# Optimization experiments

Measured on AMD Instinct MI355X. Metric: run time of the kernel, lower is better.

## Reference

```python
import jax, jax.numpy as jnp
import numpy as np

B, D, H, G, WR = 8192, 1024, 1024, 2, 64
URANKS = [64, 64]


def setup_inputs() -> dict:
    key = jax.random.key(0)
    ks = jax.random.split(key, 12)
    s = 0.1
    return {
        "x": jax.random.normal(ks[0], (B, D), jnp.float32),
        "h": jax.random.normal(ks[1], (B, H), jnp.float32),
        "c": jax.random.normal(ks[2], (B, H), jnp.float32),
        "dia_x": s * jax.random.normal(ks[3], (1, D), jnp.float32),
        "dia_h": s * jax.random.normal(ks[4], (1, H), jnp.float32),
        "Ux": s * jax.random.normal(ks[5], (D, WR), jnp.float32),
        "Vx": s * jax.random.normal(ks[6], (4 * H, WR), jnp.float32),
        "Uh_0": s * jax.random.normal(ks[7], (G, H // G, URANKS[0]), jnp.float32),
        "Vh_0": s * jax.random.normal(ks[8], (G, URANKS[0], 4 * (H // G)), jnp.float32),
        "Uh_1": s * jax.random.normal(ks[9], (G, H // G, URANKS[1]), jnp.float32),
        "Vh_1": s * jax.random.normal(ks[10], (G, URANKS[1], 4 * (H // G)), jnp.float32),
        "bias_x": jnp.ones((1, 4 * H), jnp.float32),
        "bias_h": jnp.ones((1, 4 * H), jnp.float32),
    }


def reference(x, h, c, dia_x, dia_h, Ux, Vx, Uh_0, Vh_0, Uh_1, Vh_1, bias_x, bias_h):
    Bn, Dn = x.shape
    Hn = h.shape[1]
    g = Uh_0.shape[0]
    Hg = Hn // g
    r0 = Uh_0.shape[2]

    # diagonal (vector-multiplication) paths, x-part zero-padded to hidden width
    vm_x = jnp.pad(dia_x * x, ((0, 0), (0, Hn - Dn)))          # [B, H]
    vm_h = dia_h * h                                           # [B, H]

    # low-rank input projection
    lowered_x = (x @ Ux) @ Vx.T                                # [B, 4H]

    # refined diagonal corrections subtracted from the low-rank outputs
    Vx4 = Vx.reshape(4, Hn, -1)[:, :Dn, :]                     # [4, D, wR]
    coef_x = jnp.sum(Ux[None, :, :] * Vx4, axis=-1)            # [4, D]
    vm_refined_x = jnp.pad(x[:, None, :] * coef_x[None], ((0, 0), (0, 0), (0, Hn - Dn))).reshape(Bn, 4 * Hn)

    Uh0f = Uh_0.reshape(Hn, r0)                                # [H, r0]
    Vh0f = jnp.transpose(Vh_0, (0, 2, 1)).reshape(4 * Hn, r0).reshape(4, Hn, r0)
    coef_h = jnp.sum(Uh0f[None, :, :] * Vh0f, axis=-1)         # [4, H]
    vm_refined_h = (h[:, None, :] * coef_h[None]).reshape(Bn, 4 * Hn)

    gx = lowered_x - vm_refined_x + bias_x
    xi, xf, xo, xn = jnp.split(gx, 4, axis=1)

    # grouped low-rank recurrent projection with cyclic group permutation
    hv = h.reshape(Bn, g, Hg)
    Uhs = [Uh_0, Uh_1]
    Vhs = [Vh_0, Vh_1]
    g_h = jnp.zeros((Bn, 4 * Hn), x.dtype)
    for i in range(g):
        idx = np.roll(np.arange(g), -i)                        # static permutation
        hp = hv[:, idx, :]                                     # [B, g, H/g]
        t = jnp.einsum('bgn,gnr->bgr', hp, Uhs[i])             # [B, g, r_i]
        t = jnp.einsum('bgr,grm->bgm', t, Vhs[i])              # [B, g, 4H/g]
        g_h = g_h + t.reshape(Bn, 4 * Hn)

    gh = g_h - vm_refined_h + bias_h
    hf, hi, hn, ho = jnp.split(gh, 4, axis=1)                  # note gate order differs from x

    base = vm_x + vm_h
    inputgate = jax.nn.sigmoid(xi + hi + base)
    forgetgate = jax.nn.sigmoid(xf + hf + base)
    outputgate = jax.nn.sigmoid(xo + ho + base)
    newgate = jnp.tanh(xn + hn + base)

    c_next = forgetgate * c + inputgate * newgate
    h_next = outputgate * jnp.tanh(c_next)
    return (h_next, c_next)
```

## Files before the change

### kernel.cpp

```cpp
#include <hip/hip_runtime.h>


typedef _Float16 half8 __attribute__((ext_vector_type(8)));
typedef _Float16 half4v __attribute__((ext_vector_type(4)));
typedef float f32x4 __attribute__((ext_vector_type(4)));

#define WS_U1F   0
#define WS_UH1F  131072
#define WS_W2    393216
#define WS_CX    1966080
#define WS_CH    1982464
#define WS_BB    1998848

__global__ __launch_bounds__(256) void prep_kernel(
    const float* __restrict__ Ux, const float* __restrict__ Vx,
    const float* __restrict__ Uh0, const float* __restrict__ Vh0,
    const float* __restrict__ Uh1, const float* __restrict__ Vh1,
    const float* __restrict__ dia_x, const float* __restrict__ dia_h,
    const float* __restrict__ bias_x, const float* __restrict__ bias_h,
    _Float16* __restrict__ U1f, _Float16* __restrict__ Uh1f,
    _Float16* __restrict__ W2f, float* __restrict__ cx,
    float* __restrict__ ch, float* __restrict__ bb)
{
    int e = blockIdx.x * 256 + threadIdx.x;
    if (e < 8192) {
        int lane = e & 63, ks = (e >> 6) & 31, ct = e >> 11;
        int l15 = lane & 15, quad = lane >> 4;
        half8 v8;
        #pragma unroll
        for (int jj = 0; jj < 8; ++jj) {
            int k = ks * 32 + quad * 8 + jj;
            v8[jj] = (_Float16)Ux[k * 64 + ct * 16 + l15];
        }
        *(half8*)&U1f[(size_t)e * 8] = v8;
    } else if (e < 24576) {
        int t = e - 8192;
        int lane = t & 63, ks = (t >> 6) & 15, ct = (t >> 10) & 3, j = t >> 12;
        int l15 = lane & 15, quad = lane >> 4;
        const float* src = (j & 1) ? Uh1 : Uh0;
        int g = j >> 1;
        half8 v8;
        #pragma unroll
        for (int jj = 0; jj < 8; ++jj) {
            int k = ks * 32 + quad * 8 + jj;
            v8[jj] = (_Float16)src[(g * 512 + k) * 64 + ct * 16 + l15];
        }
        *(half8*)&Uh1f[(size_t)t * 8] = v8;
    } else if (e < 122880) {
        int t = e - 24576;
        int lane = t & 63;
        int ksq  = (t >> 6) % 6;
        int ct   = (t / 384) & 63;
        int g01  = (t / 24576) & 1;
        int s    = t / 49152;
        int l15 = lane & 15, quad = lane >> 4;
        int k = ct * 16 + l15;
        int jx = s * 2 + g01;
        int m = (g01 == 0) ? (1024 + k) : k;
        half8 v8;
        #pragma unroll
        for (int jj = 0; jj < 8; ++jj) {
            int kk = ksq * 32 + quad * 8 + jj;
            int r = kk & 63, sect = kk >> 6;
            float val;
            if (sect == 0)      val = Vx[(jx * 1024 + k) * 64 + r];
            else if (sect == 1) val = Vh0[(s * 64 + r) * 2048 + m];
            else                val = Vh1[(s * 64 + r) * 2048 + m];
            v8[jj] = (_Float16)val;
        }
        *(half8*)&W2f[(size_t)t * 8] = v8;
    } else {
        int t64 = e - 122880;
        int t = t64 >> 6;
        int r = t64 & 63;
        int q = t >> 10; int k = t & 1023;
        int jh = q ^ 1;
        int fh = jh * 1024 + k; int g = fh >> 11; int m = fh & 2047;
        float sx = Ux[k * 64 + r] * Vx[(q * 1024 + k) * 64 + r];
        float sh = Uh0[k * 64 + r] * Vh0[(g * 64 + r) * 2048 + m];
        #pragma unroll
        for (int d = 32; d > 0; d >>= 1) {
            sx += __shfl_xor(sx, d, 64);
            sh += __shfl_xor(sh, d, 64);
        }
        if (r == 0) {
            cx[t] = dia_x[k] - sx;
            ch[t] = dia_h[k] - sh;
            bb[t] = bias_x[q * 1024 + k] + bias_h[jh * 1024 + k];
        }
    }
}

__global__ __launch_bounds__(512, 2) void fused_kernel(
    const float* __restrict__ x, const float* __restrict__ h,
    const float* __restrict__ c,
    const _Float16* __restrict__ U1f, const _Float16* __restrict__ Uh1f,
    const _Float16* __restrict__ W2f,
    const float* __restrict__ cx, const float* __restrict__ ch,
    const float* __restrict__ bb, float* __restrict__ out)
{
    __shared__ __align__(16) _Float16 Xsh[32][1032];
    __shared__ __align__(16) _Float16 Hsh[32][1032];
    __shared__ __align__(16) _Float16 Tsh[32][328];

    const int tid = threadIdx.x;
    const int w = tid >> 6, l = tid & 63, l15 = l & 15, quad = l >> 4;
    const int b0 = blockIdx.x * 32;
    const size_t rowbase = (size_t)b0 * 1024;

    {
        const float* xs = x + rowbase;
        const float* hs = h + rowbase;
        #pragma unroll
        for (int ii = 0; ii < 16; ++ii) {
            int idx = tid + ii * 512;
            int row = idx >> 8, c4 = idx & 255;
            float4 fx = *(const float4*)&xs[(size_t)row * 1024 + c4 * 4];
            float4 fh = *(const float4*)&hs[(size_t)row * 1024 + c4 * 4];
            half4v px, ph;
            px[0] = (_Float16)fx.x; px[1] = (_Float16)fx.y;
            px[2] = (_Float16)fx.z; px[3] = (_Float16)fx.w;
            ph[0] = (_Float16)fh.x; ph[1] = (_Float16)fh.y;
            ph[2] = (_Float16)fh.z; ph[3] = (_Float16)fh.w;
            *(half4v*)&Xsh[row][c4 * 4] = px;
            *(half4v*)&Hsh[row][c4 * 4] = ph;
        }
    }
    __syncthreads();

    {
        int rt = w & 1, ct = w >> 1;
        f32x4 acc = {};
        const _Float16* bp = U1f + ((size_t)(ct * 32) * 64 + l) * 8;
        #pragma unroll
        for (int ks = 0; ks < 32; ++ks) {
            half8 a = *(const half8*)&Xsh[rt * 16 + l15][ks * 32 + quad * 8];
            half8 b = *(const half8*)(bp + (size_t)ks * 512);
            acc = __builtin_amdgcn_mfma_f32_16x16x32_f16(a, b, acc, 0, 0, 0);
        }
        #pragma unroll
        for (int r = 0; r < 4; ++r)
            Tsh[rt * 16 + quad * 4 + r][ct * 16 + l15] = (_Float16)acc[r];

        #pragma unroll
        for (int i = 0; i < 4; ++i) {
            int p = w * 4 + i;
            int j = p >> 3, rem = p & 7, prt = rem >> 2, pct = rem & 3;
            int hoff = (j == 1 || j == 2) ? 512 : 0;
            f32x4 pa = {};
            const _Float16* pb = Uh1f + ((size_t)((j * 4 + pct) * 16) * 64 + l) * 8;
            #pragma unroll
            for (int ks = 0; ks < 16; ++ks) {
                half8 a = *(const half8*)&Hsh[prt * 16 + l15][hoff + ks * 32 + quad * 8];
                half8 b = *(const half8*)(pb + (size_t)ks * 512);
                pa = __builtin_amdgcn_mfma_f32_16x16x32_f16(a, b, pa, 0, 0, 0);
            }
            #pragma unroll
            for (int r = 0; r < 4; ++r)
                Tsh[prt * 16 + quad * 4 + r][64 + j * 64 + pct * 16 + l15] = (_Float16)pa[r];
        }
    }
    __syncthreads();

    const int secIF[3] = {0, 64, 128};
    const int secON[3] = {0, 192, 256};
    half8 Afrag[2][6][2];
    #pragma unroll
    for (int ks = 0; ks < 6; ++ks) {
        #pragma unroll
        for (int rt = 0; rt < 2; ++rt) {
            int coff = (ks & 1) * 32 + quad * 8;
            Afrag[0][ks][rt] = *(const half8*)&Tsh[rt * 16 + l15][secIF[ks >> 1] + coff];
            Afrag[1][ks][rt] = *(const half8*)&Tsh[rt * 16 + l15][secON[ks >> 1] + coff];
        }
    }

    float cpref[2][2][4];
    {
        int k0 = w * 16 + l15;
        #pragma unroll
        for (int rt = 0; rt < 2; ++rt)
            #pragma unroll
            for (int r = 0; r < 4; ++r)
                cpref[0][rt][r] = c[rowbase + (size_t)(rt * 16 + quad * 4 + r) * 1024 + k0];
    }

    #pragma unroll
    for (int i = 0; i < 8; ++i) {
        const int ctg = w + 8 * i;
        const int k = ctg * 16 + l15;

        if (i < 7) {
            int kn = (ctg + 8) * 16 + l15;
            #pragma unroll
            for (int rt = 0; rt < 2; ++rt)
                #pragma unroll
                for (int r = 0; r < 4; ++r)
                    cpref[(i + 1) & 1][rt][r] =
                        c[rowbase + (size_t)(rt * 16 + quad * 4 + r) * 1024 + kn];
        }

        float cxi = cx[k], cxf = cx[1024 + k], cxo = cx[2048 + k], cxn = cx[3072 + k];
        float chi = ch[k], chf = ch[1024 + k], cho = ch[2048 + k], chn = ch[3072 + k];
        float bbi = bb[k], bbf = bb[1024 + k], bbo = bb[2048 + k], bbn = bb[3072 + k];

        const size_t laneoff = (size_t)l * 8;
        const _Float16* bpi = W2f + (size_t)((0 * 64 + ctg) * 6) * 512 + laneoff;
        const _Float16* bpf = W2f + (size_t)((1 * 64 + ctg) * 6) * 512 + laneoff;
        const _Float16* bpo = W2f + (size_t)((2 * 64 + ctg) * 6) * 512 + laneoff;
        const _Float16* bpn = W2f + (size_t)((3 * 64 + ctg) * 6) * 512 + laneoff;

        f32x4 acc[4][2] = {};
        #pragma unroll
        for (int ks = 0; ks < 6; ++ks) {
            half8 bi = *(const half8*)(bpi + (size_t)ks * 512);
            half8 bf = *(const half8*)(bpf + (size_t)ks * 512);
            half8 bo = *(const half8*)(bpo + (size_t)ks * 512);
            half8 bn = *(const half8*)(bpn + (size_t)ks * 512);
            #pragma unroll
            for (int rt = 0; rt < 2; ++rt) {
                acc[0][rt] = __builtin_amdgcn_mfma_f32_16x16x32_f16(Afrag[0][ks][rt], bi, acc[0][rt], 0, 0, 0);
                acc[1][rt] = __builtin_amdgcn_mfma_f32_16x16x32_f16(Afrag[0][ks][rt], bf, acc[1][rt], 0, 0, 0);
                acc[2][rt] = __builtin_amdgcn_mfma_f32_16x16x32_f16(Afrag[1][ks][rt], bo, acc[2][rt], 0, 0, 0);
                acc[3][rt] = __builtin_amdgcn_mfma_f32_16x16x32_f16(Afrag[1][ks][rt], bn, acc[3][rt], 0, 0, 0);
            }
        }

        #pragma unroll
        for (int rt = 0; rt < 2; ++rt) {
            #pragma unroll
            for (int r = 0; r < 4; ++r) {
                int rl = rt * 16 + quad * 4 + r;
                size_t off = rowbase + (size_t)rl * 1024 + k;
                float xv = (float)Xsh[rl][k];
                float hv = (float)Hsh[rl][k];
                float cvv = cpref[i & 1][rt][r];
                float pi = acc[0][rt][r] + xv * cxi + hv * chi + bbi;
                float pf = acc[1][rt][r] + xv * cxf + hv * chf + bbf;
                float po = acc[2][rt][r] + xv * cxo + hv * cho + bbo;
                float pn = acc[3][rt][r] + xv * cxn + hv * chn + bbn;
                float ig = __builtin_amdgcn_rcpf(1.f + __expf(-pi));
                float fg = __builtin_amdgcn_rcpf(1.f + __expf(-pf));
                float og = __builtin_amdgcn_rcpf(1.f + __expf(-po));
                float ng = 1.f - 2.f * __builtin_amdgcn_rcpf(__expf(2.f * pn) + 1.f);
                float cn = fg * cvv + ig * ng;
                float tc = 1.f - 2.f * __builtin_amdgcn_rcpf(__expf(2.f * cn) + 1.f);
                __builtin_nontemporal_store(og * tc, &out[off]);
                __builtin_nontemporal_store(cn, &out[(size_t)8388608 + off]);
            }
        }
    }
}

extern "C" void kernel_launch(void* const* d_in, const int* in_sizes, int n_in,
                              void* d_out, int out_size, void* d_ws, size_t ws_size,
                              hipStream_t stream)
{
    const float* x      = (const float*)d_in[0];
    const float* h      = (const float*)d_in[1];
    const float* c      = (const float*)d_in[2];
    const float* dia_x  = (const float*)d_in[3];
    const float* dia_h  = (const float*)d_in[4];
    const float* Ux     = (const float*)d_in[5];
    const float* Vx     = (const float*)d_in[6];
    const float* Uh0    = (const float*)d_in[7];
    const float* Vh0    = (const float*)d_in[8];
    const float* Uh1    = (const float*)d_in[9];
    const float* Vh1    = (const float*)d_in[10];
    const float* bias_x = (const float*)d_in[11];
    const float* bias_h = (const float*)d_in[12];
    float* out = (float*)d_out;

    char* ws = (char*)d_ws;
    _Float16* U1f  = (_Float16*)(ws + WS_U1F);
    _Float16* Uh1f = (_Float16*)(ws + WS_UH1F);
    _Float16* W2f  = (_Float16*)(ws + WS_W2);
    float* cx = (float*)(ws + WS_CX);
    float* ch = (float*)(ws + WS_CH);
    float* bb = (float*)(ws + WS_BB);

    prep_kernel<<<1504, 256, 0, stream>>>(Ux, Vx, Uh0, Vh0, Uh1, Vh1,
                                          dia_x, dia_h, bias_x, bias_h,
                                          U1f, Uh1f, W2f, cx, ch, bb);
    fused_kernel<<<256, 512, 0, stream>>>(x, h, c, U1f, Uh1f, W2f,
                                          cx, ch, bb, out);
}
```

Baseline: 246.5 us.

## Use 1024-thread blocks with rebalanced wave work and nontemporal input loads

Doubles the block size of the fused kernel to 16 waves and redistributes the first-stage projection tiles and the gate-column loop across them, so each wave covers fewer columns. The A fragments of the second GEMM are now re-read from shared memory inside the loop instead of being held in registers, which lowers register pressure. Input loads of x, h and c become nontemporal, and output stores go back to ordinary stores. Occupancy drops to one block per CU, with extra LDS reads in the inner loop and an uneven per-wave split in the first stage.

```diff
diff --git a/kernel.cpp b/kernel.cpp
--- a/kernel.cpp
+++ b/kernel.cpp
@@ -91,7 +91,7 @@
     }
 }
 
-__global__ __launch_bounds__(512, 2) void fused_kernel(
+__global__ __launch_bounds__(1024) void fused_kernel(
     const float* __restrict__ x, const float* __restrict__ h,
     const float* __restrict__ c,
     const _Float16* __restrict__ U1f, const _Float16* __restrict__ Uh1f,
@@ -112,23 +112,25 @@
         const float* xs = x + rowbase;
         const float* hs = h + rowbase;
         #pragma unroll
-        for (int ii = 0; ii < 16; ++ii) {
-            int idx = tid + ii * 512;
+        for (int ii = 0; ii < 8; ++ii) {
+            int idx = tid + ii * 1024;
             int row = idx >> 8, c4 = idx & 255;
-            float4 fx = *(const float4*)&xs[(size_t)row * 1024 + c4 * 4];
-            float4 fh = *(const float4*)&hs[(size_t)row * 1024 + c4 * 4];
+            f32x4 fx = __builtin_nontemporal_load(
+                (const f32x4*)&xs[(size_t)row * 1024 + c4 * 4]);
+            f32x4 fh = __builtin_nontemporal_load(
+                (const f32x4*)&hs[(size_t)row * 1024 + c4 * 4]);
             half4v px, ph;
-            px[0] = (_Float16)fx.x; px[1] = (_Float16)fx.y;
-            px[2] = (_Float16)fx.z; px[3] = (_Float16)fx.w;
-            ph[0] = (_Float16)fh.x; ph[1] = (_Float16)fh.y;
-            ph[2] = (_Float16)fh.z; ph[3] = (_Float16)fh.w;
+            px[0] = (_Float16)fx[0]; px[1] = (_Float16)fx[1];
+            px[2] = (_Float16)fx[2]; px[3] = (_Float16)fx[3];
+            ph[0] = (_Float16)fh[0]; ph[1] = (_Float16)fh[1];
+            ph[2] = (_Float16)fh[2]; ph[3] = (_Float16)fh[3];
             *(half4v*)&Xsh[row][c4 * 4] = px;
             *(half4v*)&Hsh[row][c4 * 4] = ph;
         }
     }
     __syncthreads();
 
-    {
+    if (w < 8) {
         int rt = w & 1, ct = w >> 1;
         f32x4 acc = {};
         const _Float16* bp = U1f + ((size_t)(ct * 32) * 64 + l) * 8;
@@ -141,10 +143,13 @@
         #pragma unroll
         for (int r = 0; r < 4; ++r)
             Tsh[rt * 16 + quad * 4 + r][ct * 16 + l15] = (_Float16)acc[r];
-
-        #pragma unroll
-        for (int i = 0; i < 4; ++i) {
-            int p = w * 4 + i;
+    }
+    {
+        int pstart = (w < 8) ? w : 8 + (w - 8) * 3;
+        int pcnt   = (w < 8) ? 1 : 3;
+        for (int ii = 0; ii < 3; ++ii) {
+            if (ii >= pcnt) break;
+            int p = pstart + ii;
             int j = p >> 3, rem = p & 7, prt = rem >> 2, pct = rem & 3;
             int hoff = (j == 1 || j == 2) ? 512 : 0;
             f32x4 pa = {};
@@ -164,16 +169,6 @@
 
     const int secIF[3] = {0, 64, 128};
     const int secON[3] = {0, 192, 256};
-    half8 Afrag[2][6][2];
-    #pragma unroll
-    for (int ks = 0; ks < 6; ++ks) {
-        #pragma unroll
-        for (int rt = 0; rt < 2; ++rt) {
-            int coff = (ks & 1) * 32 + quad * 8;
-            Afrag[0][ks][rt] = *(const half8*)&Tsh[rt * 16 + l15][secIF[ks >> 1] + coff];
-            Afrag[1][ks][rt] = *(const half8*)&Tsh[rt * 16 + l15][secON[ks >> 1] + coff];
-        }
-    }
 
     float cpref[2][2][4];
     {
@@ -182,22 +177,23 @@
         for (int rt = 0; rt < 2; ++rt)
             #pragma unroll
             for (int r = 0; r < 4; ++r)
-                cpref[0][rt][r] = c[rowbase + (size_t)(rt * 16 + quad * 4 + r) * 1024 + k0];
+                cpref[0][rt][r] = __builtin_nontemporal_load(
+                    &c[rowbase + (size_t)(rt * 16 + quad * 4 + r) * 1024 + k0]);
     }
 
     #pragma unroll
-    for (int i = 0; i < 8; ++i) {
-        const int ctg = w + 8 * i;
+    for (int i = 0; i < 4; ++i) {
+        const int ctg = w + 16 * i;
         const int k = ctg * 16 + l15;
 
-        if (i < 7) {
-            int kn = (ctg + 8) * 16 + l15;
+        if (i < 3) {
+            int kn = k + 256;
             #pragma unroll
             for (int rt = 0; rt < 2; ++rt)
                 #pragma unroll
                 for (int r = 0; r < 4; ++r)
-                    cpref[(i + 1) & 1][rt][r] =
-                        c[rowbase + (size_t)(rt * 16 + quad * 4 + r) * 1024 + kn];
+                    cpref[(i + 1) & 1][rt][r] = __builtin_nontemporal_load(
+                        &c[rowbase + (size_t)(rt * 16 + quad * 4 + r) * 1024 + kn]);
         }
 
         float cxi = cx[k], cxf = cx[1024 + k], cxo = cx[2048 + k], cxn = cx[3072 + k];
@@ -217,12 +213,15 @@
             half8 bf = *(const half8*)(bpf + (size_t)ks * 512);
             half8 bo = *(const half8*)(bpo + (size_t)ks * 512);
             half8 bn = *(const half8*)(bpn + (size_t)ks * 512);
+            int coff = (ks & 1) * 32 + quad * 8;
             #pragma unroll
             for (int rt = 0; rt < 2; ++rt) {
-                acc[0][rt] = __builtin_amdgcn_mfma_f32_16x16x32_f16(Afrag[0][ks][rt], bi, acc[0][rt], 0, 0, 0);
-                acc[1][rt] = __builtin_amdgcn_mfma_f32_16x16x32_f16(Afrag[0][ks][rt], bf, acc[1][rt], 0, 0, 0);
-                acc[2][rt] = __builtin_amdgcn_mfma_f32_16x16x32_f16(Afrag[1][ks][rt], bo, acc[2][rt], 0, 0, 0);
-                acc[3][rt] = __builtin_amdgcn_mfma_f32_16x16x32_f16(Afrag[1][ks][rt], bn, acc[3][rt], 0, 0, 0);
+                half8 aA = *(const half8*)&Tsh[rt * 16 + l15][secIF[ks >> 1] + coff];
+                half8 aB = *(const half8*)&Tsh[rt * 16 + l15][secON[ks >> 1] + coff];
+                acc[0][rt] = __builtin_amdgcn_mfma_f32_16x16x32_f16(aA, bi, acc[0][rt], 0, 0, 0);
+                acc[1][rt] = __builtin_amdgcn_mfma_f32_16x16x32_f16(aA, bf, acc[1][rt], 0, 0, 0);
+                acc[2][rt] = __builtin_amdgcn_mfma_f32_16x16x32_f16(aB, bo, acc[2][rt], 0, 0, 0);
+                acc[3][rt] = __builtin_amdgcn_mfma_f32_16x16x32_f16(aB, bn, acc[3][rt], 0, 0, 0);
             }
         }
 
@@ -245,8 +244,8 @@
                 float ng = 1.f - 2.f * __builtin_amdgcn_rcpf(__expf(2.f * pn) + 1.f);
                 float cn = fg * cvv + ig * ng;
                 float tc = 1.f - 2.f * __builtin_amdgcn_rcpf(__expf(2.f * cn) + 1.f);
-                __builtin_nontemporal_store(og * tc, &out[off]);
-                __builtin_nontemporal_store(cn, &out[(size_t)8388608 + off]);
+                out[off] = og * tc;
+                out[(size_t)8388608 + off] = cn;
             }
         }
     }
@@ -282,6 +281,6 @@
     prep_kernel<<<1504, 256, 0, stream>>>(Ux, Vx, Uh0, Vh0, Uh1, Vh1,
                                           dia_x, dia_h, bias_x, bias_h,
                                           U1f, Uh1f, W2f, cx, ch, bb);
-    fused_kernel<<<256, 512, 0, stream>>>(x, h, c, U1f, Uh1f, W2f,
-                                          cx, ch, bb, out);
+    fused_kernel<<<256, 1024, 0, stream>>>(x, h, c, U1f, Uh1f, W2f,
+                                           cx, ch, bb, out);
 }
```

Result: faster. 203.2 us (-17.6%).
